# Performance work log

Measured on AMD Instinct MI355X. Metric: run time of the kernel, lower is better.

The kernel has to match this reference:

```python
import jax, jax.numpy as jnp
import numpy as np

L, B, E, H = 2048, 2, 1024, 16
HD = E // H


def setup_inputs() -> dict:
    key = jax.random.key(0)
    ks = jax.random.split(key, 7)
    return {
        "query": jax.random.normal(ks[0], (L, B, E), dtype=jnp.float32),
        "key": jax.random.normal(ks[1], (L, B, E), dtype=jnp.float32),
        "value": jax.random.normal(ks[2], (L, B, E), dtype=jnp.float32),
        "in_proj_weight": jax.random.normal(ks[3], (3 * E, E), dtype=jnp.float32) * 0.02,
        "in_proj_bias": jax.random.normal(ks[4], (3 * E,), dtype=jnp.float32) * 0.02,
        "out_proj_weight": jax.random.normal(ks[5], (E, E), dtype=jnp.float32) * 0.02,
        "out_proj_bias": jax.random.normal(ks[6], (E,), dtype=jnp.float32) * 0.02,
    }


def reference(query, key, value, in_proj_weight, in_proj_bias, out_proj_weight, out_proj_bias):
    l, b, e = query.shape
    scaling = jnp.asarray(HD, query.dtype) ** -0.5
    wq, wk, wv = jnp.split(in_proj_weight, 3, axis=0)
    bq, bk, bv = jnp.split(in_proj_bias, 3)
    q = (query @ wq.T + bq) * scaling          # [L,B,E]
    k = key @ wk.T + bk
    v = value @ wv.T + bv

    def to_heads(t):  # [L,B,E] -> [B*H, L, HD]
        return t.reshape(l, b * H, HD).transpose(1, 0, 2)

    q, k, v = to_heads(q), to_heads(k), to_heads(v)
    scores = jnp.einsum('nld,nmd->nlm', q, k)  # [B*H, L, L] materialized as in legacy MHA
    attn = jax.nn.softmax(scores, axis=-1)
    out = jnp.einsum('nlm,nmd->nld', attn, v)  # [B*H, L, HD]
    out = out.transpose(1, 0, 2).reshape(l, b, e)
    return out @ out_proj_weight.T + out_proj_bias
```

## Files before the change

### kernel.cpp

```cpp
#include <hip/hip_runtime.h>
#include <hip/hip_bf16.h>

typedef __attribute__((ext_vector_type(8))) short short8;
typedef __attribute__((ext_vector_type(4))) float floatx4;
typedef __attribute__((ext_vector_type(16))) float floatx16;

#define L_SEQ 2048
#define EMB   1024
#define HD    64
#define QSCALE 0.18033688011112042f
#define FIXMAX2 11.541560327111707f

__device__ __forceinline__ unsigned short f2bf(float f) {
    unsigned int u = __float_as_uint(f);
    u += 0x7fffu + ((u >> 16) & 1u);
    return (unsigned short)(u >> 16);
}
__device__ __forceinline__ unsigned pkbf(float a, float b) {
    return (unsigned)f2bf(a) | ((unsigned)f2bf(b) << 16);
}
__device__ __forceinline__ unsigned pkbf2(float a, float b) {
    __hip_bfloat162 h = __float22bfloat162_rn(make_float2(a, b));
    unsigned u; __builtin_memcpy(&u, &h, 4); return u;
}
__device__ __forceinline__ void gld_lds16(const void* g, void* l) {
    __builtin_amdgcn_global_load_lds(
        (const __attribute__((address_space(1))) unsigned*)g,
        (__attribute__((address_space(3))) unsigned*)l, 16, 0, 0);
}
__device__ __forceinline__ float fexp2(float x) {
    return __builtin_amdgcn_exp2f(x);
}

__global__ __launch_bounds__(256) void convert_all(
    const float* __restrict__ q, const float* __restrict__ k,
    const float* __restrict__ v, const float* __restrict__ ipw,
    const float* __restrict__ opw,
    unsigned short* __restrict__ Abq, unsigned short* __restrict__ Abk,
    unsigned short* __restrict__ Abv, unsigned short* __restrict__ Wipb,
    unsigned short* __restrict__ Wopb)
{
    const int NA = 1048576, NIP = 786432;
    int idx = blockIdx.x * 256 + threadIdx.x;
    const float* src; unsigned short* dst; int o;
    if (idx < NA)            { src = q;   dst = Abq;  o = idx; }
    else if (idx < 2 * NA)   { src = k;   dst = Abk;  o = idx - NA; }
    else if (idx < 3 * NA)   { src = v;   dst = Abv;  o = idx - 2 * NA; }
    else if (idx < 3 * NA + NIP) { src = ipw; dst = Wipb; o = idx - 3 * NA; }
    else                     { src = opw; dst = Wopb; o = idx - 3 * NA - NIP; }
    float4 f = ((const float4*)src)[o];
    ((uint2*)dst)[o] = make_uint2(pkbf(f.x, f.y), pkbf(f.z, f.w));
}

__global__ __launch_bounds__(256, 3) void qkv_gemm(
    const unsigned short* __restrict__ Abq, const unsigned short* __restrict__ Abk,
    const unsigned short* __restrict__ Abv, const unsigned short* __restrict__ Wb,
    const float* __restrict__ Bip,
    unsigned short* __restrict__ Qf, unsigned short* __restrict__ Kf,
    unsigned short* __restrict__ Vf)
{
    __shared__ unsigned short lds[17408];
    unsigned short* As = lds;
    unsigned short* Bs = lds + 8192;

    const int tid = threadIdx.x, lane = tid & 63, w = tid >> 6;
    const int wm = (w & 1) * 64, wn = (w >> 1) * 64;
    const int m0 = blockIdx.x * 128, n0 = blockIdx.y * 128;
    const int cn = lane & 15, g = lane >> 4;
    const int z = n0 >> 10;
    const unsigned short* Ag = (z == 0) ? Abq : (z == 1) ? Abk : Abv;

    floatx4 acc[4][4];
    #pragma unroll
    for (int i = 0; i < 4; ++i)
        #pragma unroll
        for (int j = 0; j < 4; ++j) acc[i][j] = (floatx4){0.f, 0.f, 0.f, 0.f};

    for (int k0 = 0; k0 < EMB; k0 += 64) {
        __syncthreads();
        #pragma unroll
        for (int p = 0; p < 4; ++p) {
            int u0 = (p * 4 + w) * 64, u = u0 + lane, row = u >> 3, sl = u & 7;
            gld_lds16(Ag + (size_t)(m0 + row) * EMB + k0 + ((sl ^ (row & 7)) * 8), &As[u0 * 8]);
            gld_lds16(Wb + (size_t)(n0 + row) * EMB + k0 + ((sl ^ (row & 7)) * 8), &Bs[u0 * 8]);
        }
        __syncthreads();
        #pragma unroll
        for (int kc = 0; kc < 2; ++kc) {
            short8 a4[4], b4[4];
            #pragma unroll
            for (int i = 0; i < 4; ++i)
                a4[i] = *(const short8*)&As[(wm + i * 16 + cn) * 64 + (((kc * 4 + g) ^ (cn & 7)) * 8)];
            #pragma unroll
            for (int j = 0; j < 4; ++j)
                b4[j] = *(const short8*)&Bs[(wn + j * 16 + cn) * 64 + (((kc * 4 + g) ^ (cn & 7)) * 8)];
            #pragma unroll
            for (int i = 0; i < 4; ++i)
                #pragma unroll
                for (int j = 0; j < 4; ++j)
                    acc[i][j] = __builtin_amdgcn_mfma_f32_16x16x32_bf16(a4[i], b4[j], acc[i][j], 0, 0, 0);
        }
    }

    const int c32l = lane & 31, hi5 = lane >> 5;
    const int b = w >> 1, hl = w & 1;

    if (z < 2) {
        __syncthreads();
        #pragma unroll
        for (int j = 0; j < 4; ++j) {
            int cl = wn + j * 16 + cn;
            float bv = Bip[n0 + cl];
            #pragma unroll
            for (int i = 0; i < 4; ++i)
                #pragma unroll
                for (int r = 0; r < 4; ++r) {
                    int rr = wm + i * 16 + g * 4 + r;
                    float vv = acc[i][j][r] + bv;
                    lds[rr * 136 + cl] = f2bf(z == 0 ? vv * QSCALE : vv);
                }
        }
        __syncthreads();
        const int h0 = (n0 & 1023) >> 6;
        const int nn = b * 16 + h0 + hl;
        unsigned short* Dst = (z == 0) ? Qf : Kf;
        #pragma unroll
        for (int cc = 0; cc < 8; ++cc) {
            int t32l = cc >> 2, kk = cc & 3;
            int rr = (t32l * 32 + c32l) * 2 + b;
            int ccol = hl * 64 + kk * 16 + hi5 * 8;
            uint4 val = *(const uint4*)&lds[rr * 136 + ccol];
            int ck = (nn * 64 + (m0 >> 6) + t32l) * 4 + kk;
            *(uint4*)(Dst + (size_t)ck * 512 + lane * 8) = val;
        }
    } else {
        __syncthreads();
        #pragma unroll
        for (int j = 0; j < 4; ++j) {
            int col_l = wn + j * 16 + cn;
            float bv = Bip[n0 + col_l];
            #pragma unroll
            for (int i = 0; i < 4; ++i) {
                int rrb = wm + i * 16 + g * 4;
                int l0 = rrb >> 1;
                float v0 = acc[i][j][0] + bv, v1 = acc[i][j][1] + bv;
                float v2 = acc[i][j][2] + bv, v3 = acc[i][j][3] + bv;
                *(unsigned*)&lds[col_l * 136 +      l0] = pkbf(v0, v2);
                *(unsigned*)&lds[col_l * 136 + 64 + l0] = pkbf(v1, v3);
            }
        }
        __syncthreads();
        const int h0 = (n0 - 2048) >> 6;
        const int nn = b * 16 + h0 + hl;
        #pragma unroll
        for (int cc = 0; cc < 8; ++cc) {
            int dt = cc >> 2, kk2l = cc & 3;
            int col_l = hl * 64 + dt * 32 + c32l;
            int keyl = kk2l * 16 + hi5 * 8;
            uint4 val = *(const uint4*)&lds[col_l * 136 + b * 64 + keyl];
            int cv = nn * 256 + ((m0 >> 5) + kk2l) * 2 + dt;
            *(uint4*)(Vf + (size_t)cv * 512 + lane * 8) = val;
        }
    }
}

__global__ __launch_bounds__(256, 2) void flash_attn_k(
    const unsigned short* __restrict__ Qf, const unsigned short* __restrict__ Kf,
    const unsigned short* __restrict__ Vf, unsigned short* __restrict__ Oh)
{
    const int id = blockIdx.y * 32 + blockIdx.x;
    const int xcd = id & 7, slot = id >> 3;
    const int n = xcd * 4 + (slot & 3);
    const int q0 = (slot >> 2) * 64;

    __shared__ float Uf[2 * 64 * 67];

    const int tid = threadIdx.x, lane = tid & 63, w = tid >> 6;
    const int c32 = lane & 31, hi = lane >> 5;

    short8 qf[2][4];
    #pragma unroll
    for (int qt = 0; qt < 2; ++qt)
        #pragma unroll
        for (int kk = 0; kk < 4; ++kk)
            qf[qt][kk] = *(const short8*)(Qf + ((size_t)((n * 64 + (q0 >> 5) + qt) * 4 + kk)) * 512 + lane * 8);

    floatx16 acc_o[2][2];
    #pragma unroll
    for (int qt = 0; qt < 2; ++qt)
        #pragma unroll
        for (int dt = 0; dt < 2; ++dt)
            #pragma unroll
            for (int r = 0; r < 16; ++r) acc_o[qt][dt][r] = 0.f;
    float lsum0 = 0.f, lsum1 = 0.f;

    const unsigned short* kp = Kf + ((size_t)n * 256 + w * 64) * 512 + lane * 8;
    const unsigned short* vp = Vf + ((size_t)n * 256 + w * 64) * 512 + lane * 8;

    for (int t = 0; t < 16; ++t) {
        short8 kf[4], vf[2][2];
        #pragma unroll
        for (int kk = 0; kk < 4; ++kk)
            kf[kk] = *(const short8*)(kp + kk * 512);
        #pragma unroll
        for (int kc = 0; kc < 2; ++kc)
            #pragma unroll
            for (int dt = 0; dt < 2; ++dt)
                vf[kc][dt] = *(const short8*)(vp + (kc * 2 + dt) * 512);
        kp += 2048; vp += 2048;

        floatx16 s[2];
        #pragma unroll
        for (int qt = 0; qt < 2; ++qt) {
            #pragma unroll
            for (int r = 0; r < 16; ++r) s[qt][r] = -FIXMAX2;
            __builtin_amdgcn_s_setprio(1);
            #pragma unroll
            for (int kk = 0; kk < 4; ++kk)
                s[qt] = __builtin_amdgcn_mfma_f32_32x32x16_bf16(kf[kk], qf[qt][kk], s[qt], 0, 0, 0);
            __builtin_amdgcn_s_setprio(0);
        }

        #pragma unroll
        for (int qt = 0; qt < 2; ++qt) {
            float p[16];
            #pragma unroll
            for (int r = 0; r < 16; ++r) p[r] = fexp2(s[qt][r]);
            float ls = ((p[0] + p[1]) + (p[2] + p[3])) + ((p[4] + p[5]) + (p[6] + p[7]))
                     + ((p[8] + p[9]) + (p[10] + p[11])) + ((p[12] + p[13]) + (p[14] + p[15]));
            if (qt == 0) lsum0 += ls; else lsum1 += ls;

            short8 pa[2];
            #pragma unroll
            for (int kc = 0; kc < 2; ++kc) {
                unsigned A = pkbf2(p[kc * 8 + 0], p[kc * 8 + 1]);
                unsigned B = pkbf2(p[kc * 8 + 2], p[kc * 8 + 3]);
                unsigned C = pkbf2(p[kc * 8 + 4], p[kc * 8 + 5]);
                unsigned D = pkbf2(p[kc * 8 + 6], p[kc * 8 + 7]);
                asm("v_permlane32_swap_b32 %0, %1" : "+v"(A), "+v"(C));
                asm("v_permlane32_swap_b32 %0, %1" : "+v"(B), "+v"(D));
                union { unsigned u[4]; short8 v; } cv;
                cv.u[0] = A; cv.u[1] = B; cv.u[2] = C; cv.u[3] = D;
                pa[kc] = cv.v;
            }

            __builtin_amdgcn_s_setprio(1);
            #pragma unroll
            for (int kc = 0; kc < 2; ++kc)
                #pragma unroll
                for (int dt = 0; dt < 2; ++dt)
                    acc_o[qt][dt] = __builtin_amdgcn_mfma_f32_32x32x16_bf16(pa[kc], vf[kc][dt], acc_o[qt][dt], 0, 0, 0);
            __builtin_amdgcn_s_setprio(0);
        }
    }

    {
        float a0 = lsum0, b0 = lsum0;
        asm("v_permlane32_swap_b32 %0, %1" : "+v"(a0), "+v"(b0));
        lsum0 = a0 + b0;
        float a1 = lsum1, b1 = lsum1;
        asm("v_permlane32_swap_b32 %0, %1" : "+v"(a1), "+v"(b1));
        lsum1 = a1 + b1;
    }

#define BLOB_STORE(base) do {                                              \
    _Pragma("unroll")                                                      \
    for (int qt = 0; qt < 2; ++qt)                                         \
        _Pragma("unroll")                                                  \
        for (int dt = 0; dt < 2; ++dt)                                     \
            _Pragma("unroll")                                              \
            for (int r = 0; r < 16; ++r)                                   \
                Uf[(base) + (qt * 2 + dt) * 16 + r] = acc_o[qt][dt][r];    \
    Uf[(base) + 64] = lsum0; Uf[(base) + 65] = lsum1;                      \
} while (0)
#define BLOB_ADD(base) do {                                                \
    _Pragma("unroll")                                                      \
    for (int qt = 0; qt < 2; ++qt)                                         \
        _Pragma("unroll")                                                  \
        for (int dt = 0; dt < 2; ++dt)                                     \
            _Pragma("unroll")                                              \
            for (int r = 0; r < 16; ++r)                                   \
                acc_o[qt][dt][r] += Uf[(base) + (qt * 2 + dt) * 16 + r];   \
    lsum0 += Uf[(base) + 64]; lsum1 += Uf[(base) + 65];                    \
} while (0)

    const int r0 = lane * 67, r1 = 64 * 67 + lane * 67;
    __syncthreads();
    if (w == 1) BLOB_STORE(r0);
    if (w == 3) BLOB_STORE(r1);
    __syncthreads();
    if (w == 0) BLOB_ADD(r0);
    if (w == 2) { BLOB_ADD(r1); BLOB_STORE(r1); }
    __syncthreads();
    if (w == 0) {
        BLOB_ADD(r1);
        float inv0 = 1.0f / lsum0, inv1 = 1.0f / lsum1;
        const int hib = hi * 16;
        const int bb = n >> 4, h = n & 15;
        #pragma unroll
        for (int qt = 0; qt < 2; ++qt) {
            float invq = qt ? inv1 : inv0;
            #pragma unroll
            for (int r = 0; r < 16; ++r) {
                int idx = ((r & 3) + 8 * (r >> 2)) * 4 + hib;
                float invr = __int_as_float(__builtin_amdgcn_ds_bpermute(idx, __float_as_int(invq)));
                int q = q0 + qt * 32 + (r & 3) + 8 * (r >> 2) + hi * 4;
                #pragma unroll
                for (int dt = 0; dt < 2; ++dt) {
                    int e = h * 64 + dt * 32 + c32;
                    Oh[((size_t)q * 2 + bb) * EMB + e] = f2bf(acc_o[qt][dt][r] * invr);
                }
            }
        }
    }
#undef BLOB_STORE
#undef BLOB_ADD
}

__global__ __launch_bounds__(256, 4) void out_gemm(
    const unsigned short* __restrict__ Oh, const unsigned short* __restrict__ Wob,
    const float* __restrict__ bo, float* __restrict__ out)
{
    __shared__ unsigned short As[64 * 64];
    __shared__ unsigned short Bs[128 * 64];

    const int tid = threadIdx.x, lane = tid & 63, w = tid >> 6;
    const int wm = (w & 1) * 32, wn = (w >> 1) * 64;
    const int m0 = blockIdx.x * 64, n0 = blockIdx.y * 128;
    const int cn = lane & 15, g = lane >> 4;

    floatx4 acc[2][4];
    #pragma unroll
    for (int i = 0; i < 2; ++i)
        #pragma unroll
        for (int j = 0; j < 4; ++j) acc[i][j] = (floatx4){0.f, 0.f, 0.f, 0.f};

    for (int k0 = 0; k0 < EMB; k0 += 64) {
        __syncthreads();
        #pragma unroll
        for (int p = 0; p < 4; ++p) {
            int u0 = (p * 4 + w) * 64, u = u0 + lane, row = u >> 3, sl = u & 7;
            if (p < 2)
                gld_lds16(Oh + (size_t)(m0 + row) * EMB + k0 + ((sl ^ (row & 7)) * 8), &As[u0 * 8]);
            gld_lds16(Wob + (size_t)(n0 + row) * EMB + k0 + ((sl ^ (row & 7)) * 8), &Bs[u0 * 8]);
        }
        __syncthreads();
        #pragma unroll
        for (int kc = 0; kc < 2; ++kc) {
            short8 a4[2], b4[4];
            #pragma unroll
            for (int i = 0; i < 2; ++i)
                a4[i] = *(const short8*)&As[(wm + i * 16 + cn) * 64 + (((kc * 4 + g) ^ (cn & 7)) * 8)];
            #pragma unroll
            for (int j = 0; j < 4; ++j)
                b4[j] = *(const short8*)&Bs[(wn + j * 16 + cn) * 64 + (((kc * 4 + g) ^ (cn & 7)) * 8)];
            #pragma unroll
            for (int i = 0; i < 2; ++i)
                #pragma unroll
                for (int j = 0; j < 4; ++j)
                    acc[i][j] = __builtin_amdgcn_mfma_f32_16x16x32_bf16(a4[i], b4[j], acc[i][j], 0, 0, 0);
        }
    }

    #pragma unroll
    for (int j = 0; j < 4; ++j) {
        int col = n0 + wn + j * 16 + cn;
        float bv = bo[col];
        #pragma unroll
        for (int i = 0; i < 2; ++i)
            #pragma unroll
            for (int r = 0; r < 4; ++r)
                out[(size_t)(m0 + wm + i * 16 + g * 4 + r) * EMB + col] = acc[i][j][r] + bv;
    }
}

extern "C" void kernel_launch(void* const* d_in, const int* in_sizes, int n_in,
                              void* d_out, int out_size, void* d_ws, size_t ws_size,
                              hipStream_t stream) {
    const float* q   = (const float*)d_in[0];
    const float* k   = (const float*)d_in[1];
    const float* v   = (const float*)d_in[2];
    const float* ipw = (const float*)d_in[3];
    const float* ipb = (const float*)d_in[4];
    const float* opw = (const float*)d_in[5];
    const float* opb = (const float*)d_in[6];
    float* out = (float*)d_out;

    const size_t HE = (size_t)32 * L_SEQ * HD;
    unsigned short* Qf   = (unsigned short*)d_ws;
    unsigned short* Kf   = Qf + HE;
    unsigned short* Vf   = Kf + HE;
    unsigned short* Wipb = Vf + HE;
    unsigned short* Wopb = Wipb + (size_t)3 * EMB * EMB;
    unsigned short* Abq  = Wopb + (size_t)EMB * EMB;
    unsigned short* Abk  = Abq + HE;
    unsigned short* Abv  = Abk + HE;
    unsigned short* Oh   = Abq;

    convert_all<<<dim3(16384), 256, 0, stream>>>(q, k, v, ipw, opw, Abq, Abk, Abv, Wipb, Wopb);
    qkv_gemm<<<dim3(32, 24), 256, 0, stream>>>(Abq, Abk, Abv, Wipb, ipb, Qf, Kf, Vf);
    flash_attn_k<<<dim3(32, 32), 256, 0, stream>>>(Qf, Kf, Vf, Oh);
    out_gemm<<<dim3(64, 8), 256, 0, stream>>>(Oh, Wopb, opb, out);
}
```

Before: 207.2 us.

## Double-buffer K/V fragment loads and serialize split-K reduction to halve LDS

The attention inner loop is restructured into a ping-pong scheme with two register sets of K/V fragments, so the next tile's global loads are issued before the current tile's MFMA and exp work. This is meant to hide global load latency behind compute. Separately, the cross-wave reduction buffer is halved and the reduction becomes a serial chain (wave 3 to 2 to 1 to 0) with an extra barrier. The smaller LDS footprint may help occupancy, at the cost of more VGPRs for the second fragment set and a longer epilogue.

Measured after the change: 200.8 us. 1.03x faster.

```diff
diff --git a/kernel.cpp b/kernel.cpp
--- a/kernel.cpp
+++ b/kernel.cpp
@@ -173,7 +173,7 @@
     const int n = xcd * 4 + (slot & 3);
     const int q0 = (slot >> 2) * 64;
 
-    __shared__ float Uf[2 * 64 * 67];
+    __shared__ float Uf[64 * 67];
 
     const int tid = threadIdx.x, lane = tid & 63, w = tid >> 6;
     const int c32 = lane & 31, hi = lane >> 5;
@@ -194,65 +194,75 @@
             for (int r = 0; r < 16; ++r) acc_o[qt][dt][r] = 0.f;
     float lsum0 = 0.f, lsum1 = 0.f;
 
-    const unsigned short* kp = Kf + ((size_t)n * 256 + w * 64) * 512 + lane * 8;
-    const unsigned short* vp = Vf + ((size_t)n * 256 + w * 64) * 512 + lane * 8;
-
-    for (int t = 0; t < 16; ++t) {
-        short8 kf[4], vf[2][2];
-        #pragma unroll
-        for (int kk = 0; kk < 4; ++kk)
-            kf[kk] = *(const short8*)(kp + kk * 512);
-        #pragma unroll
-        for (int kc = 0; kc < 2; ++kc)
-            #pragma unroll
-            for (int dt = 0; dt < 2; ++dt)
-                vf[kc][dt] = *(const short8*)(vp + (kc * 2 + dt) * 512);
-        kp += 2048; vp += 2048;
-
-        floatx16 s[2];
-        #pragma unroll
-        for (int qt = 0; qt < 2; ++qt) {
-            #pragma unroll
-            for (int r = 0; r < 16; ++r) s[qt][r] = -FIXMAX2;
-            __builtin_amdgcn_s_setprio(1);
-            #pragma unroll
-            for (int kk = 0; kk < 4; ++kk)
-                s[qt] = __builtin_amdgcn_mfma_f32_32x32x16_bf16(kf[kk], qf[qt][kk], s[qt], 0, 0, 0);
-            __builtin_amdgcn_s_setprio(0);
-        }
-
-        #pragma unroll
-        for (int qt = 0; qt < 2; ++qt) {
-            float p[16];
-            #pragma unroll
-            for (int r = 0; r < 16; ++r) p[r] = fexp2(s[qt][r]);
-            float ls = ((p[0] + p[1]) + (p[2] + p[3])) + ((p[4] + p[5]) + (p[6] + p[7]))
-                     + ((p[8] + p[9]) + (p[10] + p[11])) + ((p[12] + p[13]) + (p[14] + p[15]));
-            if (qt == 0) lsum0 += ls; else lsum1 += ls;
-
-            short8 pa[2];
-            #pragma unroll
-            for (int kc = 0; kc < 2; ++kc) {
-                unsigned A = pkbf2(p[kc * 8 + 0], p[kc * 8 + 1]);
-                unsigned B = pkbf2(p[kc * 8 + 2], p[kc * 8 + 3]);
-                unsigned C = pkbf2(p[kc * 8 + 4], p[kc * 8 + 5]);
-                unsigned D = pkbf2(p[kc * 8 + 6], p[kc * 8 + 7]);
-                asm("v_permlane32_swap_b32 %0, %1" : "+v"(A), "+v"(C));
-                asm("v_permlane32_swap_b32 %0, %1" : "+v"(B), "+v"(D));
-                union { unsigned u[4]; short8 v; } cv;
-                cv.u[0] = A; cv.u[1] = B; cv.u[2] = C; cv.u[3] = D;
-                pa[kc] = cv.v;
-            }
-
-            __builtin_amdgcn_s_setprio(1);
-            #pragma unroll
-            for (int kc = 0; kc < 2; ++kc)
-                #pragma unroll
-                for (int dt = 0; dt < 2; ++dt)
-                    acc_o[qt][dt] = __builtin_amdgcn_mfma_f32_32x32x16_bf16(pa[kc], vf[kc][dt], acc_o[qt][dt], 0, 0, 0);
-            __builtin_amdgcn_s_setprio(0);
-        }
-    }
+    const unsigned short* kbase = Kf + ((size_t)n * 256 + w * 64) * 512 + lane * 8;
+    const unsigned short* vbase = Vf + ((size_t)n * 256 + w * 64) * 512 + lane * 8;
+
+#define FLOAD(KF, VF, T) do {                                               \
+    const unsigned short* _kp = kbase + (size_t)(T) * 2048;                 \
+    const unsigned short* _vp = vbase + (size_t)(T) * 2048;                 \
+    _Pragma("unroll")                                                       \
+    for (int kk = 0; kk < 4; ++kk)                                          \
+        KF[kk] = *(const short8*)(_kp + kk * 512);                          \
+    _Pragma("unroll")                                                       \
+    for (int kc = 0; kc < 2; ++kc)                                          \
+        _Pragma("unroll")                                                   \
+        for (int dt = 0; dt < 2; ++dt)                                      \
+            VF[kc][dt] = *(const short8*)(_vp + (kc * 2 + dt) * 512);       \
+} while (0)
+
+#define FCOMP(KF, VF) do {                                                  \
+    floatx16 s_[2];                                                         \
+    _Pragma("unroll")                                                       \
+    for (int qt = 0; qt < 2; ++qt) {                                        \
+        _Pragma("unroll")                                                   \
+        for (int r = 0; r < 16; ++r) s_[qt][r] = -FIXMAX2;                  \
+        __builtin_amdgcn_s_setprio(1);                                      \
+        _Pragma("unroll")                                                   \
+        for (int kk = 0; kk < 4; ++kk)                                      \
+            s_[qt] = __builtin_amdgcn_mfma_f32_32x32x16_bf16(KF[kk], qf[qt][kk], s_[qt], 0, 0, 0); \
+        __builtin_amdgcn_s_setprio(0);                                      \
+    }                                                                       \
+    _Pragma("unroll")                                                       \
+    for (int qt = 0; qt < 2; ++qt) {                                        \
+        float p_[16];                                                       \
+        _Pragma("unroll")                                                   \
+        for (int r = 0; r < 16; ++r) p_[r] = fexp2(s_[qt][r]);              \
+        float ls_ = ((p_[0] + p_[1]) + (p_[2] + p_[3])) + ((p_[4] + p_[5]) + (p_[6] + p_[7])) \
+                  + ((p_[8] + p_[9]) + (p_[10] + p_[11])) + ((p_[12] + p_[13]) + (p_[14] + p_[15])); \
+        if (qt == 0) lsum0 += ls_; else lsum1 += ls_;                       \
+        short8 pa_[2];                                                      \
+        _Pragma("unroll")                                                   \
+        for (int kc = 0; kc < 2; ++kc) {                                    \
+            unsigned A_ = pkbf2(p_[kc * 8 + 0], p_[kc * 8 + 1]);            \
+            unsigned B_ = pkbf2(p_[kc * 8 + 2], p_[kc * 8 + 3]);            \
+            unsigned C_ = pkbf2(p_[kc * 8 + 4], p_[kc * 8 + 5]);            \
+            unsigned D_ = pkbf2(p_[kc * 8 + 6], p_[kc * 8 + 7]);            \
+            asm("v_permlane32_swap_b32 %0, %1" : "+v"(A_), "+v"(C_));       \
+            asm("v_permlane32_swap_b32 %0, %1" : "+v"(B_), "+v"(D_));       \
+            union { unsigned u[4]; short8 v; } cv_;                         \
+            cv_.u[0] = A_; cv_.u[1] = B_; cv_.u[2] = C_; cv_.u[3] = D_;     \
+            pa_[kc] = cv_.v;                                                \
+        }                                                                   \
+        __builtin_amdgcn_s_setprio(1);                                      \
+        _Pragma("unroll")                                                   \
+        for (int kc = 0; kc < 2; ++kc)                                      \
+            _Pragma("unroll")                                               \
+            for (int dt = 0; dt < 2; ++dt)                                  \
+                acc_o[qt][dt] = __builtin_amdgcn_mfma_f32_32x32x16_bf16(pa_[kc], VF[kc][dt], acc_o[qt][dt], 0, 0, 0); \
+        __builtin_amdgcn_s_setprio(0);                                      \
+    }                                                                       \
+} while (0)
+
+    short8 kfA[4], vfA[2][2], kfB[4], vfB[2][2];
+    FLOAD(kfA, vfA, 0);
+    for (int t = 0; t < 16; t += 2) {
+        FLOAD(kfB, vfB, t + 1);
+        FCOMP(kfA, vfA);
+        if (t + 2 < 16) FLOAD(kfA, vfA, t + 2);
+        FCOMP(kfB, vfB);
+    }
+#undef FLOAD
+#undef FCOMP
 
     {
         float a0 = lsum0, b0 = lsum0;
@@ -263,37 +273,37 @@
         lsum1 = a1 + b1;
     }
 
-#define BLOB_STORE(base) do {                                              \
+#define BLOB_STORE() do {                                                  \
     _Pragma("unroll")                                                      \
     for (int qt = 0; qt < 2; ++qt)                                         \
         _Pragma("unroll")                                                  \
         for (int dt = 0; dt < 2; ++dt)                                     \
             _Pragma("unroll")                                              \
             for (int r = 0; r < 16; ++r)                                   \
-                Uf[(base) + (qt * 2 + dt) * 16 + r] = acc_o[qt][dt][r];    \
-    Uf[(base) + 64] = lsum0; Uf[(base) + 65] = lsum1;                      \
+                Uf[ub + (qt * 2 + dt) * 16 + r] = acc_o[qt][dt][r];        \
+    Uf[ub + 64] = lsum0; Uf[ub + 65] = lsum1;                              \
 } while (0)
-#define BLOB_ADD(base) do {                                                \
+#define BLOB_ADD() do {                                                    \
     _Pragma("unroll")                                                      \
     for (int qt = 0; qt < 2; ++qt)                                         \
         _Pragma("unroll")                                                  \
         for (int dt = 0; dt < 2; ++dt)                                     \
             _Pragma("unroll")                                              \
             for (int r = 0; r < 16; ++r)                                   \
-                acc_o[qt][dt][r] += Uf[(base) + (qt * 2 + dt) * 16 + r];   \
-    lsum0 += Uf[(base) + 64]; lsum1 += Uf[(base) + 65];                    \
+                acc_o[qt][dt][r] += Uf[ub + (qt * 2 + dt) * 16 + r];       \
+    lsum0 += Uf[ub + 64]; lsum1 += Uf[ub + 65];                            \
 } while (0)
 
-    const int r0 = lane * 67, r1 = 64 * 67 + lane * 67;
+    const int ub = lane * 67;
     __syncthreads();
-    if (w == 1) BLOB_STORE(r0);
-    if (w == 3) BLOB_STORE(r1);
+    if (w == 3) BLOB_STORE();
     __syncthreads();
-    if (w == 0) BLOB_ADD(r0);
-    if (w == 2) { BLOB_ADD(r1); BLOB_STORE(r1); }
+    if (w == 2) { BLOB_ADD(); BLOB_STORE(); }
+    __syncthreads();
+    if (w == 1) { BLOB_ADD(); BLOB_STORE(); }
     __syncthreads();
     if (w == 0) {
-        BLOB_ADD(r1);
+        BLOB_ADD();
         float inv0 = 1.0f / lsum0, inv1 = 1.0f / lsum1;
         const int hib = hi * 16;
         const int bb = n >> 4, h = n & 15;
```
